# Performance work log

Measured on AMD Instinct MI355X. Metric: run time of the kernel, lower is better.

The kernel has to match this reference:

```python
import jax, jax.numpy as jnp
import numpy as np

PAD = 0
CONST_NO = 10000   # ids > CONST_NO are variables
N_PRED = 50
B, S, G = 8, 64, 8
F, R, BMAX = 200000, 200, 3
K_F, K_R = 64, 32  # max fact / rule children per state


def _is_var(x):
    return x > CONST_NO


def setup_inputs() -> dict:
    key = jax.random.key(0)
    ks = jax.random.split(key, 12)
    # facts: (pred, arg0, arg1), preds in [1, N_PRED], args are constants
    fp = jax.random.randint(ks[0], (F, 1), 1, N_PRED + 1, dtype=jnp.int32)
    fa = jax.random.randint(ks[1], (F, 2), 1, CONST_NO + 1, dtype=jnp.int32)
    facts = jnp.concatenate([fp, fa], axis=1)
    fact_scores = jax.random.uniform(ks[2], (F,), jnp.float32, 0.1, 1.0)
    # rule heads: p(V1, V2) with V1 = CONST_NO+1, V2 = CONST_NO+2
    hp = jax.random.randint(ks[3], (R, 1), 1, N_PRED + 1, dtype=jnp.int32)
    heads = jnp.concatenate([hp,
                             jnp.full((R, 1), CONST_NO + 1, jnp.int32),
                             jnp.full((R, 1), CONST_NO + 2, jnp.int32)], axis=1)
    # rule bodies: args are head vars or fresh constants
    bp = jax.random.randint(ks[4], (R, BMAX, 1), 1, N_PRED + 1, dtype=jnp.int32)
    choice = jax.random.randint(ks[5], (R, BMAX, 2), 0, 3, dtype=jnp.int32)
    consts = jax.random.randint(ks[6], (R, BMAX, 2), 1, CONST_NO + 1, dtype=jnp.int32)
    bargs = jnp.where(choice == 0, CONST_NO + 1,
                      jnp.where(choice == 1, CONST_NO + 2, consts)).astype(jnp.int32)
    bodies = jnp.concatenate([bp, bargs], axis=2)
    rule_lens = jax.random.randint(ks[7], (R,), 1, BMAX + 1, dtype=jnp.int32)
    rule_scores = jax.random.uniform(ks[8], (R,), jnp.float32, 0.1, 1.0)
    # proof goals [B,S,G,3]: args mix of constants and query vars CONST_NO+3/+4
    gp = jax.random.randint(ks[9], (B, S, G, 1), 1, N_PRED + 1, dtype=jnp.int32)
    vch = jax.random.randint(ks[10], (B, S, G, 2), 0, 4, dtype=jnp.int32)
    gc = jax.random.randint(ks[11], (B, S, G, 2), 1, CONST_NO + 1, dtype=jnp.int32)
    gargs = jnp.where(vch == 0, CONST_NO + 3,
                      jnp.where(vch == 1, CONST_NO + 4, gc)).astype(jnp.int32)
    goals = jnp.concatenate([gp, gargs], axis=3)
    # variable number of live goals per state (tail padded)
    pos = jnp.arange(G)
    keep = jax.random.randint(jax.random.fold_in(key, 99), (B, S, 1), 1, G + 1, dtype=jnp.int32)
    goals = jnp.where(pos[None, None, :, None] < keep[..., None], goals, PAD)
    state_scores = jax.random.uniform(jax.random.fold_in(key, 7), (B, S), jnp.float32, 0.1, 1.0)
    return dict(proof_goals=goals, state_scores=state_scores, facts=facts,
                fact_scores=fact_scores, heads=heads, bodies=bodies,
                rule_lens=rule_lens, rule_scores=rule_scores)


def reference(proof_goals, state_scores, facts, fact_scores, heads, bodies, rule_lens, rule_scores):
    # ---- 1. SELECT: query = goal slot 0, remaining goals mask slot 0 ----
    q = proof_goals[:, :, 0]                         # [B,S,3]
    active = q[..., 0] != PAD                        # [B,S]
    remaining = proof_goals.at[:, :, 0, :].set(PAD)  # [B,S,G,3]
    qp, qa0, qa1 = q[..., 0], q[..., 1], q[..., 2]

    # ---- 2. RESOLVE FACTS: unify query against fact table ----
    m = ((qp[..., None] == facts[:, 0])
         & (_is_var(qa0)[..., None] | (qa0[..., None] == facts[:, 1]))
         & (_is_var(qa1)[..., None] | (qa1[..., None] == facts[:, 2]))
         & active[..., None])                        # [B,S,F]
    fvals, fidx = jax.lax.top_k(m.astype(jnp.int32), K_F)
    fact_success = fvals > 0                         # [B,S,K_f]
    mf = facts[fidx]                                 # [B,S,K_f,3]
    # substitute query variables with matched fact constants in remaining goals
    v0 = qa0[:, :, None, None, None]
    v1 = qa1[:, :, None, None, None]
    b0 = mf[..., 1][..., None, None]
    b1 = mf[..., 2][..., None, None]
    rem = remaining[:, :, None]                      # [B,S,1,G,3]
    fg = jnp.where(_is_var(v0) & (rem == v0), b0, rem)
    fg = jnp.where(_is_var(v1) & (fg == v1), b1, fg)  # [B,S,K_f,G,3]
    fsc = jnp.where(fact_success, state_scores[:, :, None] * fact_scores[fidx], 0.0)

    # ---- 3. RESOLVE RULES: unify query against rule heads, append bodies ----
    mr = ((qp[..., None] == heads[:, 0])
          & (_is_var(heads[:, 1]) | _is_var(qa0)[..., None] | (qa0[..., None] == heads[:, 1]))
          & (_is_var(heads[:, 2]) | _is_var(qa1)[..., None] | (qa1[..., None] == heads[:, 2]))
          & active[..., None])                       # [B,S,R]
    rvals, ridx = jax.lax.top_k(mr.astype(jnp.int32), K_R)
    rule_success = rvals > 0                         # [B,S,K_r]
    mh = heads[ridx]                                 # [B,S,K_r,3]
    body = bodies[ridx]                              # [B,S,K_r,BMAX,3]
    h0 = mh[..., 1][..., None, None]
    h1 = mh[..., 2][..., None, None]
    qa0b = qa0[:, :, None, None, None]
    qa1b = qa1[:, :, None, None, None]
    body = jnp.where(_is_var(h0) & (body == h0), qa0b, body)
    body = jnp.where(_is_var(h1) & (body == h1), qa1b, body)
    bmask = jnp.arange(BMAX) < rule_lens[ridx][..., None]    # [B,S,K_r,BMAX]
    body = jnp.where(bmask[..., None], body, PAD)
    rem_rest = jnp.broadcast_to(remaining[:, :, None, 1:1 + (G - BMAX)], (B, S, K_R, G - BMAX, 3))
    rg = jnp.concatenate([body, rem_rest], axis=3)   # [B,S,K_r,G,3]
    rsc = jnp.where(rule_success, state_scores[:, :, None] * rule_scores[ridx], 0.0)

    # ---- 4. PACK: flatten SxK children, compact successful ones to S states ----
    K = K_F + K_R
    all_goals = jnp.concatenate([fg, rg], axis=2).reshape(B, S * K, G, 3)
    all_succ = jnp.concatenate([fact_success, rule_success], axis=2).reshape(B, S * K)
    all_sc = jnp.concatenate([fsc, rsc], axis=2).reshape(B, S * K)
    pvals, pidx = jax.lax.top_k(all_succ.astype(jnp.int32), S)
    new_succ = pvals > 0                             # [B,S]
    new_goals = jnp.take_along_axis(all_goals, pidx[..., None, None], axis=1)
    # ---- 5. POSTPROCESS: zero out failed / padded states ----
    new_goals = jnp.where(new_succ[..., None, None], new_goals, PAD)
    new_scores = jnp.where(new_succ, jnp.take_along_axis(all_sc, pidx, axis=1), 0.0)
    return new_goals, new_scores
```

## Files before the change

kernel.cpp:

```cpp
#include <hip/hip_runtime.h>

#define PAD 0
#define CONST_NO 10000
#define Bn 8
#define Sn 64
#define Gn 8
#define Fn 200000
#define Rn 200
#define BMAXn 3
#define KF 64
#define KR 32

#define NBLK 196
#define CHB  1024

#define OFF_CNTF   0
#define OFF_PN     512
#define OFF_PFIRST 1024
#define OFF_UF     5120

__device__ __forceinline__ bool isv(int x) { return x > CONST_NO; }

__global__ __launch_bounds__(256) void probe_kernel(
    const int* __restrict__ goals, const int* __restrict__ facts,
    int* __restrict__ ws)
{
    const int t = threadIdx.x;
    const int lane = t & 63, wv = t >> 6;

    if (blockIdx.x < NBLK) {
        __shared__ int4 qlist[512];
        __shared__ int qcnt[64], qstart[64];
        const int B = blockIdx.x;

        if (t < 64) qcnt[t] = 0;
        __syncthreads();

        int myPos[2], myQp[2], myQv[2], myQm[2], mySt[2];
        #pragma unroll
        for (int k = 0; k < 2; ++k) {
            const int s = t + k * 256;
            const int* q = goals + s * (Gn * 3);
            const int qp = q[0], qa0 = q[1], qa1 = q[2];
            const bool v0 = isv(qa0), v1 = isv(qa1);
            const bool use = (qp != PAD) && !(v0 && v1);
            myQp[k] = use ? qp : -1;
            myQv[k] = (v0 ? 0 : (qa0 << 14)) | (v1 ? 0 : qa1);
            myQm[k] = (v0 ? 0 : (0x3FFF << 14)) | (v1 ? 0 : 0x3FFF);
            mySt[k] = s;
            myPos[k] = use ? atomicAdd(&qcnt[qp], 1) : -1;
        }
        __syncthreads();
        if (t < 64) {
            const int v = qcnt[t];
            int incl = v;
            #pragma unroll
            for (int off = 1; off < 64; off <<= 1) {
                int n = __shfl_up(incl, off, 64);
                if (t >= off) incl += n;
            }
            qstart[t] = incl - v;
        }
        __syncthreads();
        #pragma unroll
        for (int k = 0; k < 2; ++k)
            if (myQp[k] >= 0)
                qlist[qstart[myQp[k]] + myPos[k]] =
                    make_int4(myQv[k], myQm[k], mySt[k], 0);
        __syncthreads();

        const int f0 = B * CHB + t * 4;
        int pv[4], pk[4];
        if (f0 + 3 < Fn) {
            const int4* p4 = (const int4*)(facts + 3 * f0);
            int4 a = p4[0], b4 = p4[1], c4 = p4[2];
            pv[0] = a.x;  pk[0] = (a.y  << 14) | a.z;
            pv[1] = a.w;  pk[1] = (b4.x << 14) | b4.y;
            pv[2] = b4.z; pk[2] = (b4.w << 14) | c4.x;
            pv[3] = c4.y; pk[3] = (c4.z << 14) | c4.w;
        } else {
            #pragma unroll
            for (int u = 0; u < 4; ++u) {
                pv[u] = -1; pk[u] = 0;
                if (f0 + u < Fn) {
                    pv[u] = facts[3 * (f0 + u)];
                    pk[u] = (facts[3 * (f0 + u) + 1] << 14) | facts[3 * (f0 + u) + 2];
                }
            }
        }
        #pragma unroll
        for (int u = 0; u < 4; ++u) {
            if (pv[u] >= 0) {
                const int j0 = qstart[pv[u]], j1 = j0 + qcnt[pv[u]];
                for (int j = j0; j < j1; ++j) {
                    const int4 qq = qlist[j];
                    if (((pk[u] ^ qq.x) & qq.y) == 0) {
                        const int pos = atomicAdd(ws + OFF_CNTF + qq.z, 1);
                        if (pos < KF) ws[OFF_UF + qq.z * KF + pos] = f0 + u;
                    }
                }
            }
        }
    } else {
        __shared__ int wave_tot[4];
        const int p = blockIdx.x - NBLK + 1;

        int total = 0;
        for (int base = 0; base < Fn && total < KF; base += 1024) {
            const int f0 = base + t * 4;
            unsigned mbits = 0;
            if (f0 + 3 < Fn) {
                const int4* p4 = (const int4*)(facts + 3 * f0);
                int4 a = p4[0], b4 = p4[1], c4 = p4[2];
                if (a.x  == p) mbits |= 1u;
                if (a.w  == p) mbits |= 2u;
                if (b4.z == p) mbits |= 4u;
                if (c4.y == p) mbits |= 8u;
            } else {
                #pragma unroll
                for (int u = 0; u < 4; ++u)
                    if (f0 + u < Fn && facts[3 * (f0 + u)] == p) mbits |= (1u << u);
            }
            const int c4n = __popc(mbits);

            int v = c4n;
            #pragma unroll
            for (int off = 1; off < 64; off <<= 1) {
                int n = __shfl_up(v, off, 64);
                if (lane >= off) v += n;
            }
            if (lane == 63) wave_tot[wv] = v;
            __syncthreads();
            int excl = v - c4n;
            #pragma unroll
            for (int w = 0; w < 4; ++w) if (w < wv) excl += wave_tot[w];
            const int ctot = wave_tot[0] + wave_tot[1] + wave_tot[2] + wave_tot[3];

            int pos = total + excl;
            #pragma unroll
            for (int u = 0; u < 4; ++u) {
                if (mbits & (1u << u)) {
                    if (pos < KF) ws[OFF_PFIRST + p * 64 + pos] = f0 + u;
                    pos++;
                }
            }
            total += ctot;
            __syncthreads();
        }
        if (t == 0) ws[OFF_PN + p] = (total < KF) ? total : KF;
    }
}

__global__ __launch_bounds__(256) void finalize_kernel(
    const int* __restrict__ goals, const float* __restrict__ ss,
    const int* __restrict__ facts, const float* __restrict__ fsc,
    const int* __restrict__ heads, const int* __restrict__ bodies,
    const int* __restrict__ rlens, const float* __restrict__ rsc,
    const int* __restrict__ ws, float* __restrict__ outp)
{
    __shared__ int sfx[Sn * 64];
    __shared__ int seg[4][Sn][16];
    __shared__ int segc[4][Sn];
    __shared__ int hds[Rn * 3];
    __shared__ int pref[Sn + 1];
    __shared__ int nfs[Sn], nrs[Sn], vvf[Sn], qps[Sn];

    const int b = blockIdx.x, t = threadIdx.x;
    const int lane = t & 63, wv = t >> 6;

    for (int k = t; k < Rn * 3; k += 256) hds[k] = heads[k];
    segc[wv][lane] = 0;
    __syncthreads();

    {
        const int s = lane;
        const int* q = goals + (b * Sn + s) * (Gn * 3);
        const int qp = q[0], qa0 = q[1], qa1 = q[2];
        const bool v0 = isv(qa0), v1 = isv(qa1);
        const bool active = (qp != PAD);
        int cnt = 0;
        const int r0 = wv * 50;
        for (int r = r0; r < r0 + 50; ++r) {
            const int h0 = hds[3 * r], h1 = hds[3 * r + 1], h2 = hds[3 * r + 2];
            if (active && h0 == qp && (isv(h1) || v0 || qa0 == h1)
                                   && (isv(h2) || v1 || qa1 == h2)) {
                if (cnt < 16) seg[wv][s][cnt] = r;
                cnt++;
            }
        }
        segc[wv][s] = (cnt < 16) ? cnt : 16;
    }
    __syncthreads();

    if (t < Sn) {
        const int s = t;
        const int* q = goals + (b * Sn + s) * (Gn * 3);
        const int qp = q[0], qa0 = q[1], qa1 = q[2];
        const bool v0 = isv(qa0), v1 = isv(qa1);
        const bool active = (qp != PAD);
        const bool vv = active && v0 && v1;
        int nf = 0;
        if (vv) {
            nf = ws[OFF_PN + qp];
        } else if (active) {
            int c = ws[OFF_CNTF + b * Sn + s];
            if (c > KF) c = KF;
            for (int j = 0; j < c; ++j)
                sfx[s * 64 + j] = ws[OFF_UF + (b * Sn + s) * KF + j];
            for (int a = 1; a < c; ++a) {
                const int key = sfx[s * 64 + a];
                int m = a - 1;
                while (m >= 0 && sfx[s * 64 + m] > key) {
                    sfx[s * 64 + m + 1] = sfx[s * 64 + m];
                    m--;
                }
                sfx[s * 64 + m + 1] = key;
            }
            nf = c;
        }
        nfs[s] = nf;
        vvf[s] = vv ? 1 : 0;
        qps[s] = qp;
        int nr = segc[0][s] + segc[1][s] + segc[2][s] + segc[3][s];
        if (nr > KR) nr = KR;
        nrs[s] = nr;

        int incl = nf + nr;
        #pragma unroll
        for (int off = 1; off < 64; off <<= 1) {
            int n = __shfl_up(incl, off, 64);
            if (t >= off) incl += n;
        }
        pref[s + 1] = incl;
        if (s == 0) pref[0] = 0;
    }
    __syncthreads();
    const int total = pref[Sn];

    for (int item = t; item < Sn * Gn; item += 256) {
        const int i = item >> 3, g = item & 7;
        int trip[3] = {PAD, PAD, PAD};
        if (i < total) {
            int lo = 0, hi = Sn - 1;
            while (lo < hi) {
                const int mid = (lo + hi) >> 1;
                if (pref[mid + 1] <= i) lo = mid + 1; else hi = mid;
            }
            const int s = lo, j = i - pref[s];
            const int* q = goals + (b * Sn + s) * (Gn * 3);
            const int qa0 = q[1], qa1 = q[2];
            if (j < nfs[s]) {
                const int fi = vvf[s] ? ws[OFF_PFIRST + qps[s] * 64 + j]
                                      : sfx[s * 64 + j];
                const int f1 = facts[3 * fi + 1], f2 = facts[3 * fi + 2];
                if (g >= 1) {
                    #pragma unroll
                    for (int c = 0; c < 3; ++c) {
                        int x = q[g * 3 + c];
                        if (isv(qa0) && x == qa0) x = f1;
                        else if (isv(qa1) && x == qa1) x = f2;
                        trip[c] = x;
                    }
                }
            } else {
                int jr = j - nfs[s];
                int wz = 0;
                while (jr >= segc[wz][s]) { jr -= segc[wz][s]; wz++; }
                const int ri = seg[wz][s][jr];
                const int h1 = hds[3 * ri + 1], h2 = hds[3 * ri + 2];
                const int len = rlens[ri];
                if (g < BMAXn) {
                    if (g < len) {
                        #pragma unroll
                        for (int c = 0; c < 3; ++c) {
                            int x = bodies[(ri * BMAXn + g) * 3 + c];
                            if (isv(h1) && x == h1) x = qa0;
                            if (isv(h2) && x == h2) x = qa1;
                            trip[c] = x;
                        }
                    }
                } else {
                    trip[0] = q[(g - 2) * 3 + 0];
                    trip[1] = q[(g - 2) * 3 + 1];
                    trip[2] = q[(g - 2) * 3 + 2];
                }
            }
        }
        float* o = outp + ((b * Sn + i) * Gn + g) * 3;
        o[0] = (float)trip[0];
        o[1] = (float)trip[1];
        o[2] = (float)trip[2];
    }

    if (t < Sn) {
        const int i = t;
        float sc = 0.f;
        if (i < total) {
            int lo = 0, hi = Sn - 1;
            while (lo < hi) {
                const int mid = (lo + hi) >> 1;
                if (pref[mid + 1] <= i) lo = mid + 1; else hi = mid;
            }
            const int s = lo, j = i - pref[s];
            const float stt = ss[b * Sn + s];
            if (j < nfs[s]) {
                const int fi = vvf[s] ? ws[OFF_PFIRST + qps[s] * 64 + j]
                                      : sfx[s * 64 + j];
                sc = stt * fsc[fi];
            } else {
                int jr = j - nfs[s];
                int wz = 0;
                while (jr >= segc[wz][s]) { jr -= segc[wz][s]; wz++; }
                sc = stt * rsc[seg[wz][s][jr]];
            }
        }
        outp[Bn * Sn * Gn * 3 + b * Sn + t] = sc;
    }
}

extern "C" void kernel_launch(void* const* d_in, const int* in_sizes, int n_in,
                              void* d_out, int out_size, void* d_ws, size_t ws_size,
                              hipStream_t stream) {
    const int*   goals  = (const int*)  d_in[0];
    const float* ss     = (const float*)d_in[1];
    const int*   facts  = (const int*)  d_in[2];
    const float* fsc    = (const float*)d_in[3];
    const int*   heads  = (const int*)  d_in[4];
    const int*   bodies = (const int*)  d_in[5];
    const int*   rlens  = (const int*)  d_in[6];
    const float* rsc    = (const float*)d_in[7];
    int*   ws   = (int*)d_ws;
    float* outp = (float*)d_out;

    hipMemsetAsync(ws, 0, 512 * sizeof(int), stream);
    probe_kernel   <<<NBLK + 50, 256, 0, stream>>>(goals, facts, ws);
    finalize_kernel<<<Bn,        256, 0, stream>>>(goals, ss, facts, fsc, heads,
                                                   bodies, rlens, rsc, ws, outp);
}
```

Before: 90.47 us.

## Fuse memset, probe and finalize into one cooperative kernel with grid syncs

Replaces the memset plus two kernel launches with a single cooperative kernel. The workspace counters are zeroed in-kernel and the probe and finalize phases are separated by grid.sync barriers. This is meant to remove launch overhead and the gaps between the three stream operations. In exchange it adds two grid-wide barriers and cooperative launch overhead, and it raises per-block shared memory because all phases' arrays now live in one kernel, which could limit occupancy.

```diff
diff --git a/kernel.cpp b/kernel.cpp
--- a/kernel.cpp
+++ b/kernel.cpp
@@ -1,4 +1,7 @@
 #include <hip/hip_runtime.h>
+#include <hip/hip_cooperative_groups.h>
+
+namespace cg = cooperative_groups;
 
 #define PAD 0
 #define CONST_NO 10000
@@ -21,16 +24,28 @@
 
 __device__ __forceinline__ bool isv(int x) { return x > CONST_NO; }
 
-__global__ __launch_bounds__(256) void probe_kernel(
-    const int* __restrict__ goals, const int* __restrict__ facts,
-    int* __restrict__ ws)
+__global__ __launch_bounds__(256) void fused_kernel(
+    const int* __restrict__ goals, const float* __restrict__ ss,
+    const int* __restrict__ facts, const float* __restrict__ fsc,
+    const int* __restrict__ heads, const int* __restrict__ bodies,
+    const int* __restrict__ rlens, const float* __restrict__ rsc,
+    int* __restrict__ ws, float* __restrict__ outp)
 {
+    cg::grid_group grid = cg::this_grid();
     const int t = threadIdx.x;
     const int lane = t & 63, wv = t >> 6;
 
+    {
+        const int gid = blockIdx.x * 256 + t;
+        if (gid < 512) ws[OFF_CNTF + gid] = 0;
+    }
+    grid.sync();
+
+    __shared__ int4 qlist[512];
+    __shared__ int qcnt[64], qstart[64];
+    __shared__ int wave_tot[4];
+
     if (blockIdx.x < NBLK) {
-        __shared__ int4 qlist[512];
-        __shared__ int qcnt[64], qstart[64];
         const int B = blockIdx.x;
 
         if (t < 64) qcnt[t] = 0;
@@ -102,7 +117,6 @@
             }
         }
     } else {
-        __shared__ int wave_tot[4];
         const int p = blockIdx.x - NBLK + 1;
 
         int total = 0;
@@ -149,172 +163,168 @@
         }
         if (t == 0) ws[OFF_PN + p] = (total < KF) ? total : KF;
     }
-}
-
-__global__ __launch_bounds__(256) void finalize_kernel(
-    const int* __restrict__ goals, const float* __restrict__ ss,
-    const int* __restrict__ facts, const float* __restrict__ fsc,
-    const int* __restrict__ heads, const int* __restrict__ bodies,
-    const int* __restrict__ rlens, const float* __restrict__ rsc,
-    const int* __restrict__ ws, float* __restrict__ outp)
-{
-    __shared__ int sfx[Sn * 64];
-    __shared__ int seg[4][Sn][16];
-    __shared__ int segc[4][Sn];
-    __shared__ int hds[Rn * 3];
-    __shared__ int pref[Sn + 1];
-    __shared__ int nfs[Sn], nrs[Sn], vvf[Sn], qps[Sn];
-
-    const int b = blockIdx.x, t = threadIdx.x;
-    const int lane = t & 63, wv = t >> 6;
-
-    for (int k = t; k < Rn * 3; k += 256) hds[k] = heads[k];
-    segc[wv][lane] = 0;
-    __syncthreads();
-
-    {
-        const int s = lane;
-        const int* q = goals + (b * Sn + s) * (Gn * 3);
-        const int qp = q[0], qa0 = q[1], qa1 = q[2];
-        const bool v0 = isv(qa0), v1 = isv(qa1);
-        const bool active = (qp != PAD);
-        int cnt = 0;
-        const int r0 = wv * 50;
-        for (int r = r0; r < r0 + 50; ++r) {
-            const int h0 = hds[3 * r], h1 = hds[3 * r + 1], h2 = hds[3 * r + 2];
-            if (active && h0 == qp && (isv(h1) || v0 || qa0 == h1)
-                                   && (isv(h2) || v1 || qa1 == h2)) {
-                if (cnt < 16) seg[wv][s][cnt] = r;
-                cnt++;
-            }
-        }
-        segc[wv][s] = (cnt < 16) ? cnt : 16;
-    }
-    __syncthreads();
-
-    if (t < Sn) {
-        const int s = t;
-        const int* q = goals + (b * Sn + s) * (Gn * 3);
-        const int qp = q[0], qa0 = q[1], qa1 = q[2];
-        const bool v0 = isv(qa0), v1 = isv(qa1);
-        const bool active = (qp != PAD);
-        const bool vv = active && v0 && v1;
-        int nf = 0;
-        if (vv) {
-            nf = ws[OFF_PN + qp];
-        } else if (active) {
-            int c = ws[OFF_CNTF + b * Sn + s];
-            if (c > KF) c = KF;
-            for (int j = 0; j < c; ++j)
-                sfx[s * 64 + j] = ws[OFF_UF + (b * Sn + s) * KF + j];
-            for (int a = 1; a < c; ++a) {
-                const int key = sfx[s * 64 + a];
-                int m = a - 1;
-                while (m >= 0 && sfx[s * 64 + m] > key) {
-                    sfx[s * 64 + m + 1] = sfx[s * 64 + m];
-                    m--;
-                }
-                sfx[s * 64 + m + 1] = key;
-            }
-            nf = c;
-        }
-        nfs[s] = nf;
-        vvf[s] = vv ? 1 : 0;
-        qps[s] = qp;
-        int nr = segc[0][s] + segc[1][s] + segc[2][s] + segc[3][s];
-        if (nr > KR) nr = KR;
-        nrs[s] = nr;
-
-        int incl = nf + nr;
-        #pragma unroll
-        for (int off = 1; off < 64; off <<= 1) {
-            int n = __shfl_up(incl, off, 64);
-            if (t >= off) incl += n;
-        }
-        pref[s + 1] = incl;
-        if (s == 0) pref[0] = 0;
-    }
-    __syncthreads();
-    const int total = pref[Sn];
-
-    for (int item = t; item < Sn * Gn; item += 256) {
-        const int i = item >> 3, g = item & 7;
-        int trip[3] = {PAD, PAD, PAD};
-        if (i < total) {
-            int lo = 0, hi = Sn - 1;
-            while (lo < hi) {
-                const int mid = (lo + hi) >> 1;
-                if (pref[mid + 1] <= i) lo = mid + 1; else hi = mid;
-            }
-            const int s = lo, j = i - pref[s];
+
+    __threadfence();
+    grid.sync();
+
+    if (blockIdx.x < Bn) {
+        __shared__ int sfx[Sn * 64];
+        __shared__ int seg[4][Sn][16];
+        __shared__ int segc[4][Sn];
+        __shared__ int hds[Rn * 3];
+        __shared__ int pref[Sn + 1];
+        __shared__ int nfs[Sn], nrs[Sn], vvf[Sn], qps[Sn];
+
+        const int b = blockIdx.x;
+
+        for (int k = t; k < Rn * 3; k += 256) hds[k] = heads[k];
+        segc[wv][lane] = 0;
+        __syncthreads();
+
+        {
+            const int s = lane;
             const int* q = goals + (b * Sn + s) * (Gn * 3);
-            const int qa0 = q[1], qa1 = q[2];
-            if (j < nfs[s]) {
-                const int fi = vvf[s] ? ws[OFF_PFIRST + qps[s] * 64 + j]
-                                      : sfx[s * 64 + j];
-                const int f1 = facts[3 * fi + 1], f2 = facts[3 * fi + 2];
-                if (g >= 1) {
-                    #pragma unroll
-                    for (int c = 0; c < 3; ++c) {
-                        int x = q[g * 3 + c];
-                        if (isv(qa0) && x == qa0) x = f1;
-                        else if (isv(qa1) && x == qa1) x = f2;
-                        trip[c] = x;
+            const int qp = q[0], qa0 = q[1], qa1 = q[2];
+            const bool v0 = isv(qa0), v1 = isv(qa1);
+            const bool active = (qp != PAD);
+            int cnt = 0;
+            const int r0 = wv * 50;
+            for (int r = r0; r < r0 + 50; ++r) {
+                const int h0 = hds[3 * r], h1 = hds[3 * r + 1], h2 = hds[3 * r + 2];
+                if (active && h0 == qp && (isv(h1) || v0 || qa0 == h1)
+                                       && (isv(h2) || v1 || qa1 == h2)) {
+                    if (cnt < 16) seg[wv][s][cnt] = r;
+                    cnt++;
+                }
+            }
+            segc[wv][s] = (cnt < 16) ? cnt : 16;
+        }
+        __syncthreads();
+
+        if (t < Sn) {
+            const int s = t;
+            const int* q = goals + (b * Sn + s) * (Gn * 3);
+            const int qp = q[0], qa0 = q[1], qa1 = q[2];
+            const bool v0 = isv(qa0), v1 = isv(qa1);
+            const bool active = (qp != PAD);
+            const bool vv = active && v0 && v1;
+            int nf = 0;
+            if (vv) {
+                nf = ws[OFF_PN + qp];
+            } else if (active) {
+                int c = ws[OFF_CNTF + b * Sn + s];
+                if (c > KF) c = KF;
+                for (int j = 0; j < c; ++j)
+                    sfx[s * 64 + j] = ws[OFF_UF + (b * Sn + s) * KF + j];
+                for (int a = 1; a < c; ++a) {
+                    const int key = sfx[s * 64 + a];
+                    int m = a - 1;
+                    while (m >= 0 && sfx[s * 64 + m] > key) {
+                        sfx[s * 64 + m + 1] = sfx[s * 64 + m];
+                        m--;
                     }
-                }
-            } else {
-                int jr = j - nfs[s];
-                int wz = 0;
-                while (jr >= segc[wz][s]) { jr -= segc[wz][s]; wz++; }
-                const int ri = seg[wz][s][jr];
-                const int h1 = hds[3 * ri + 1], h2 = hds[3 * ri + 2];
-                const int len = rlens[ri];
-                if (g < BMAXn) {
-                    if (g < len) {
+                    sfx[s * 64 + m + 1] = key;
+                }
+                nf = c;
+            }
+            nfs[s] = nf;
+            vvf[s] = vv ? 1 : 0;
+            qps[s] = qp;
+            int nr = segc[0][s] + segc[1][s] + segc[2][s] + segc[3][s];
+            if (nr > KR) nr = KR;
+            nrs[s] = nr;
+
+            int incl = nf + nr;
+            #pragma unroll
+            for (int off = 1; off < 64; off <<= 1) {
+                int n = __shfl_up(incl, off, 64);
+                if (t >= off) incl += n;
+            }
+            pref[s + 1] = incl;
+            if (s == 0) pref[0] = 0;
+        }
+        __syncthreads();
+        const int total = pref[Sn];
+
+        for (int item = t; item < Sn * Gn; item += 256) {
+            const int i = item >> 3, g = item & 7;
+            int trip[3] = {PAD, PAD, PAD};
+            if (i < total) {
+                int lo = 0, hi = Sn - 1;
+                while (lo < hi) {
+                    const int mid = (lo + hi) >> 1;
+                    if (pref[mid + 1] <= i) lo = mid + 1; else hi = mid;
+                }
+                const int s = lo, j = i - pref[s];
+                const int* q = goals + (b * Sn + s) * (Gn * 3);
+                const int qa0 = q[1], qa1 = q[2];
+                if (j < nfs[s]) {
+                    const int fi = vvf[s] ? ws[OFF_PFIRST + qps[s] * 64 + j]
+                                          : sfx[s * 64 + j];
+                    const int f1 = facts[3 * fi + 1], f2 = facts[3 * fi + 2];
+                    if (g >= 1) {
                         #pragma unroll
                         for (int c = 0; c < 3; ++c) {
-                            int x = bodies[(ri * BMAXn + g) * 3 + c];
-                            if (isv(h1) && x == h1) x = qa0;
-                            if (isv(h2) && x == h2) x = qa1;
+                            int x = q[g * 3 + c];
+                            if (isv(qa0) && x == qa0) x = f1;
+                            else if (isv(qa1) && x == qa1) x = f2;
                             trip[c] = x;
                         }
                     }
                 } else {
-                    trip[0] = q[(g - 2) * 3 + 0];
-                    trip[1] = q[(g - 2) * 3 + 1];
-                    trip[2] = q[(g - 2) * 3 + 2];
-                }
-            }
-        }
-        float* o = outp + ((b * Sn + i) * Gn + g) * 3;
-        o[0] = (float)trip[0];
-        o[1] = (float)trip[1];
-        o[2] = (float)trip[2];
-    }
-
-    if (t < Sn) {
-        const int i = t;
-        float sc = 0.f;
-        if (i < total) {
-            int lo = 0, hi = Sn - 1;
-            while (lo < hi) {
-                const int mid = (lo + hi) >> 1;
-                if (pref[mid + 1] <= i) lo = mid + 1; else hi = mid;
-            }
-            const int s = lo, j = i - pref[s];
-            const float stt = ss[b * Sn + s];
-            if (j < nfs[s]) {
-                const int fi = vvf[s] ? ws[OFF_PFIRST + qps[s] * 64 + j]
-                                      : sfx[s * 64 + j];
-                sc = stt * fsc[fi];
-            } else {
-                int jr = j - nfs[s];
-                int wz = 0;
-                while (jr >= segc[wz][s]) { jr -= segc[wz][s]; wz++; }
-                sc = stt * rsc[seg[wz][s][jr]];
-            }
-        }
-        outp[Bn * Sn * Gn * 3 + b * Sn + t] = sc;
+                    int jr = j - nfs[s];
+                    int wz = 0;
+                    while (jr >= segc[wz][s]) { jr -= segc[wz][s]; wz++; }
+                    const int ri = seg[wz][s][jr];
+                    const int h1 = hds[3 * ri + 1], h2 = hds[3 * ri + 2];
+                    const int len = rlens[ri];
+                    if (g < BMAXn) {
+                        if (g < len) {
+                            #pragma unroll
+                            for (int c = 0; c < 3; ++c) {
+                                int x = bodies[(ri * BMAXn + g) * 3 + c];
+                                if (isv(h1) && x == h1) x = qa0;
+                                if (isv(h2) && x == h2) x = qa1;
+                                trip[c] = x;
+                            }
+                        }
+                    } else {
+                        trip[0] = q[(g - 2) * 3 + 0];
+                        trip[1] = q[(g - 2) * 3 + 1];
+                        trip[2] = q[(g - 2) * 3 + 2];
+                    }
+                }
+            }
+            float* o = outp + ((b * Sn + i) * Gn + g) * 3;
+            o[0] = (float)trip[0];
+            o[1] = (float)trip[1];
+            o[2] = (float)trip[2];
+        }
+
+        if (t < Sn) {
+            const int i = t;
+            float sc = 0.f;
+            if (i < total) {
+                int lo = 0, hi = Sn - 1;
+                while (lo < hi) {
+                    const int mid = (lo + hi) >> 1;
+                    if (pref[mid + 1] <= i) lo = mid + 1; else hi = mid;
+                }
+                const int s = lo, j = i - pref[s];
+                const float stt = ss[b * Sn + s];
+                if (j < nfs[s]) {
+                    const int fi = vvf[s] ? ws[OFF_PFIRST + qps[s] * 64 + j]
+                                          : sfx[s * 64 + j];
+                    sc = stt * fsc[fi];
+                } else {
+                    int jr = j - nfs[s];
+                    int wz = 0;
+                    while (jr >= segc[wz][s]) { jr -= segc[wz][s]; wz++; }
+                    sc = stt * rsc[seg[wz][s][jr]];
+                }
+            }
+            outp[Bn * Sn * Gn * 3 + b * Sn + t] = sc;
+        }
     }
 }
 
@@ -332,8 +342,11 @@
     int*   ws   = (int*)d_ws;
     float* outp = (float*)d_out;
 
-    hipMemsetAsync(ws, 0, 512 * sizeof(int), stream);
-    probe_kernel   <<<NBLK + 50, 256, 0, stream>>>(goals, facts, ws);
-    finalize_kernel<<<Bn,        256, 0, stream>>>(goals, ss, facts, fsc, heads,
-                                                   bodies, rlens, rsc, ws, outp);
+    void* args[] = {
+        (void*)&goals, (void*)&ss, (void*)&facts, (void*)&fsc,
+        (void*)&heads, (void*)&bodies, (void*)&rlens, (void*)&rsc,
+        (void*)&ws, (void*)&outp
+    };
+    hipLaunchCooperativeKernel((void*)fused_kernel, dim3(NBLK + 50), dim3(256),
+                               args, 0, stream);
 }
```

Result: slower. 162.0 us (+79.0%).

## Build goal index once in setup kernel, replacing memset and per-block rebuild

Applied to the files above, without the earlier changes.

Goal bucketing (qlist/qstart/qcnt) used to be recomputed in every probe block; it is now built once by block 0 of a new setup kernel and stored in workspace. The same block zeroes the match counters, so the separate hipMemsetAsync is dropped. The per-predicate first-fact scan moves into the setup kernel. The probe kernel now just loads the prebuilt index. This removes redundant per-block shared-memory index building, but the probe must now wait for the setup kernel, so the first-fact scan no longer overlaps with probing.

```diff
diff --git a/kernel.cpp b/kernel.cpp
--- a/kernel.cpp
+++ b/kernel.cpp
@@ -18,21 +18,25 @@
 #define OFF_PN     512
 #define OFF_PFIRST 1024
 #define OFF_UF     5120
+#define OFF_QSTART 37888
+#define OFF_QCNT   37952
+#define OFF_QLIST  38016
 
 __device__ __forceinline__ bool isv(int x) { return x > CONST_NO; }
 
-__global__ __launch_bounds__(256) void probe_kernel(
+__global__ __launch_bounds__(256) void setup_kernel(
     const int* __restrict__ goals, const int* __restrict__ facts,
     int* __restrict__ ws)
 {
     const int t = threadIdx.x;
     const int lane = t & 63, wv = t >> 6;
 
-    if (blockIdx.x < NBLK) {
+    if (blockIdx.x == 0) {
+        ws[OFF_CNTF + t] = 0;
+        ws[OFF_CNTF + 256 + t] = 0;
+
         __shared__ int4 qlist[512];
         __shared__ int qcnt[64], qstart[64];
-        const int B = blockIdx.x;
-
         if (t < 64) qcnt[t] = 0;
         __syncthreads();
 
@@ -69,41 +73,16 @@
                     make_int4(myQv[k], myQm[k], mySt[k], 0);
         __syncthreads();
 
-        const int f0 = B * CHB + t * 4;
-        int pv[4], pk[4];
-        if (f0 + 3 < Fn) {
-            const int4* p4 = (const int4*)(facts + 3 * f0);
-            int4 a = p4[0], b4 = p4[1], c4 = p4[2];
-            pv[0] = a.x;  pk[0] = (a.y  << 14) | a.z;
-            pv[1] = a.w;  pk[1] = (b4.x << 14) | b4.y;
-            pv[2] = b4.z; pk[2] = (b4.w << 14) | c4.x;
-            pv[3] = c4.y; pk[3] = (c4.z << 14) | c4.w;
-        } else {
-            #pragma unroll
-            for (int u = 0; u < 4; ++u) {
-                pv[u] = -1; pk[u] = 0;
-                if (f0 + u < Fn) {
-                    pv[u] = facts[3 * (f0 + u)];
-                    pk[u] = (facts[3 * (f0 + u) + 1] << 14) | facts[3 * (f0 + u) + 2];
-                }
-            }
-        }
-        #pragma unroll
-        for (int u = 0; u < 4; ++u) {
-            if (pv[u] >= 0) {
-                const int j0 = qstart[pv[u]], j1 = j0 + qcnt[pv[u]];
-                for (int j = j0; j < j1; ++j) {
-                    const int4 qq = qlist[j];
-                    if (((pk[u] ^ qq.x) & qq.y) == 0) {
-                        const int pos = atomicAdd(ws + OFF_CNTF + qq.z, 1);
-                        if (pos < KF) ws[OFF_UF + qq.z * KF + pos] = f0 + u;
-                    }
-                }
-            }
-        }
+        if (t < 64) {
+            ws[OFF_QSTART + t] = qstart[t];
+            ws[OFF_QCNT + t]   = qcnt[t];
+        }
+        int4* dst = (int4*)(ws + OFF_QLIST);
+        dst[t]       = qlist[t];
+        dst[t + 256] = qlist[t + 256];
     } else {
         __shared__ int wave_tot[4];
-        const int p = blockIdx.x - NBLK + 1;
+        const int p = blockIdx.x;
 
         int total = 0;
         for (int base = 0; base < Fn && total < KF; base += 1024) {
@@ -151,6 +130,59 @@
     }
 }
 
+__global__ __launch_bounds__(256) void probe_kernel(
+    const int* __restrict__ facts, int* __restrict__ ws)
+{
+    __shared__ int4 qlist[512];
+    __shared__ int qstart[64], qcnt[64];
+    const int t = threadIdx.x;
+    const int B = blockIdx.x;
+
+    {
+        const int4* src = (const int4*)(ws + OFF_QLIST);
+        qlist[t]       = src[t];
+        qlist[t + 256] = src[t + 256];
+        if (t < 64) {
+            qstart[t] = ws[OFF_QSTART + t];
+            qcnt[t]   = ws[OFF_QCNT + t];
+        }
+    }
+    __syncthreads();
+
+    const int f0 = B * CHB + t * 4;
+    int pv[4], pk[4];
+    if (f0 + 3 < Fn) {
+        const int4* p4 = (const int4*)(facts + 3 * f0);
+        int4 a = p4[0], b4 = p4[1], c4 = p4[2];
+        pv[0] = a.x;  pk[0] = (a.y  << 14) | a.z;
+        pv[1] = a.w;  pk[1] = (b4.x << 14) | b4.y;
+        pv[2] = b4.z; pk[2] = (b4.w << 14) | c4.x;
+        pv[3] = c4.y; pk[3] = (c4.z << 14) | c4.w;
+    } else {
+        #pragma unroll
+        for (int u = 0; u < 4; ++u) {
+            pv[u] = -1; pk[u] = 0;
+            if (f0 + u < Fn) {
+                pv[u] = facts[3 * (f0 + u)];
+                pk[u] = (facts[3 * (f0 + u) + 1] << 14) | facts[3 * (f0 + u) + 2];
+            }
+        }
+    }
+    #pragma unroll
+    for (int u = 0; u < 4; ++u) {
+        if (pv[u] >= 0) {
+            const int j0 = qstart[pv[u]], j1 = j0 + qcnt[pv[u]];
+            for (int j = j0; j < j1; ++j) {
+                const int4 qq = qlist[j];
+                if (((pk[u] ^ qq.x) & qq.y) == 0) {
+                    const int pos = atomicAdd(ws + OFF_CNTF + qq.z, 1);
+                    if (pos < KF) ws[OFF_UF + qq.z * KF + pos] = f0 + u;
+                }
+            }
+        }
+    }
+}
+
 __global__ __launch_bounds__(256) void finalize_kernel(
     const int* __restrict__ goals, const float* __restrict__ ss,
     const int* __restrict__ facts, const float* __restrict__ fsc,
@@ -163,7 +195,7 @@
     __shared__ int segc[4][Sn];
     __shared__ int hds[Rn * 3];
     __shared__ int pref[Sn + 1];
-    __shared__ int nfs[Sn], nrs[Sn], vvf[Sn], qps[Sn];
+    __shared__ int nfs[Sn], vvf[Sn], qps[Sn];
 
     const int b = blockIdx.x, t = threadIdx.x;
     const int lane = t & 63, wv = t >> 6;
@@ -223,7 +255,6 @@
         qps[s] = qp;
         int nr = segc[0][s] + segc[1][s] + segc[2][s] + segc[3][s];
         if (nr > KR) nr = KR;
-        nrs[s] = nr;
 
         int incl = nf + nr;
         #pragma unroll
@@ -332,8 +363,8 @@
     int*   ws   = (int*)d_ws;
     float* outp = (float*)d_out;
 
-    hipMemsetAsync(ws, 0, 512 * sizeof(int), stream);
-    probe_kernel   <<<NBLK + 50, 256, 0, stream>>>(goals, facts, ws);
-    finalize_kernel<<<Bn,        256, 0, stream>>>(goals, ss, facts, fsc, heads,
-                                                   bodies, rlens, rsc, ws, outp);
+    setup_kernel   <<<51,   256, 0, stream>>>(goals, facts, ws);
+    probe_kernel   <<<NBLK, 256, 0, stream>>>(facts, ws);
+    finalize_kernel<<<Bn,   256, 0, stream>>>(goals, ss, facts, fsc, heads,
+                                              bodies, rlens, rsc, ws, outp);
 }
```

Result: slower. 96.31 us (+6.4%).

## Replace global atomic fact-match lists with per-block compacted buffers, drop memset

Applied to the files above, without the earlier changes.

The probe kernel no longer does a global atomicAdd per matching fact. Each block counts its matches, takes a block-wide prefix scan and writes packed (state, fact) entries into its own buffer region. The finalize kernel gathers all block buffers into shared memory, and each state scans the whole entry list to collect its facts in fact order. That ordering makes the insertion sort unnecessary. Removing the per-launch hipMemsetAsync drops one stream operation, but the match loop now runs twice and every state does a linear scan over up to 2048 entries.

```diff
diff --git a/kernel.cpp b/kernel.cpp
--- a/kernel.cpp
+++ b/kernel.cpp
@@ -13,11 +13,13 @@
 
 #define NBLK 196
 #define CHB  1024
-
-#define OFF_CNTF   0
-#define OFF_PN     512
-#define OFF_PFIRST 1024
-#define OFF_UF     5120
+#define CAP  1024
+#define ENTCAP 2048
+
+#define OFF_PN     0
+#define OFF_PFIRST 64
+#define OFF_BCNT   4160
+#define OFF_GBUF   4360
 
 __device__ __forceinline__ bool isv(int x) { return x > CONST_NO; }
 
@@ -31,12 +33,13 @@
     if (blockIdx.x < NBLK) {
         __shared__ int4 qlist[512];
         __shared__ int qcnt[64], qstart[64];
+        __shared__ int wtot[4];
         const int B = blockIdx.x;
 
         if (t < 64) qcnt[t] = 0;
         __syncthreads();
 
-        int myPos[2], myQp[2], myQv[2], myQm[2], mySt[2];
+        int myPos[2], myQp[2], myQv[2], myQm[2];
         #pragma unroll
         for (int k = 0; k < 2; ++k) {
             const int s = t + k * 256;
@@ -47,7 +50,6 @@
             myQp[k] = use ? qp : -1;
             myQv[k] = (v0 ? 0 : (qa0 << 14)) | (v1 ? 0 : qa1);
             myQm[k] = (v0 ? 0 : (0x3FFF << 14)) | (v1 ? 0 : 0x3FFF);
-            mySt[k] = s;
             myPos[k] = use ? atomicAdd(&qcnt[qp], 1) : -1;
         }
         __syncthreads();
@@ -66,7 +68,7 @@
         for (int k = 0; k < 2; ++k)
             if (myQp[k] >= 0)
                 qlist[qstart[myQp[k]] + myPos[k]] =
-                    make_int4(myQv[k], myQm[k], mySt[k], 0);
+                    make_int4(myQv[k], myQm[k], t + k * 256, 0);
         __syncthreads();
 
         const int f0 = B * CHB + t * 4;
@@ -88,15 +90,46 @@
                 }
             }
         }
+
+        int myCnt = 0;
         #pragma unroll
         for (int u = 0; u < 4; ++u) {
             if (pv[u] >= 0) {
                 const int j0 = qstart[pv[u]], j1 = j0 + qcnt[pv[u]];
                 for (int j = j0; j < j1; ++j) {
                     const int4 qq = qlist[j];
-                    if (((pk[u] ^ qq.x) & qq.y) == 0) {
-                        const int pos = atomicAdd(ws + OFF_CNTF + qq.z, 1);
-                        if (pos < KF) ws[OFF_UF + qq.z * KF + pos] = f0 + u;
+                    if (((pk[u] ^ qq.x) & qq.y) == 0) myCnt++;
+                }
+            }
+        }
+
+        int incl = myCnt;
+        #pragma unroll
+        for (int off = 1; off < 64; off <<= 1) {
+            int n = __shfl_up(incl, off, 64);
+            if (lane >= off) incl += n;
+        }
+        if (lane == 63) wtot[wv] = incl;
+        __syncthreads();
+        int excl = incl - myCnt;
+        #pragma unroll
+        for (int w = 0; w < 4; ++w) if (w < wv) excl += wtot[w];
+        const int btot = wtot[0] + wtot[1] + wtot[2] + wtot[3];
+        if (t == 0) ws[OFF_BCNT + B] = (btot < CAP) ? btot : CAP;
+
+        if (myCnt > 0) {
+            int* dst = ws + OFF_GBUF + B * CAP;
+            int k = excl;
+            #pragma unroll
+            for (int u = 0; u < 4; ++u) {
+                if (pv[u] >= 0) {
+                    const int j0 = qstart[pv[u]], j1 = j0 + qcnt[pv[u]];
+                    for (int j = j0; j < j1; ++j) {
+                        const int4 qq = qlist[j];
+                        if (((pk[u] ^ qq.x) & qq.y) == 0) {
+                            if (k < CAP) dst[k] = (qq.z << 18) | (f0 + u);
+                            k++;
+                        }
                     }
                 }
             }
@@ -163,14 +196,41 @@
     __shared__ int segc[4][Sn];
     __shared__ int hds[Rn * 3];
     __shared__ int pref[Sn + 1];
-    __shared__ int nfs[Sn], nrs[Sn], vvf[Sn], qps[Sn];
+    __shared__ int nfs[Sn], vvf[Sn], qps[Sn];
+    __shared__ int ent[ENTCAP];
+    __shared__ int bco[NBLK];
+    __shared__ int wsum[4];
 
     const int b = blockIdx.x, t = threadIdx.x;
     const int lane = t & 63, wv = t >> 6;
 
     for (int k = t; k < Rn * 3; k += 256) hds[k] = heads[k];
     segc[wv][lane] = 0;
+
+    const int bc = (t < NBLK) ? ws[OFF_BCNT + t] : 0;
+    int binc = bc;
+    #pragma unroll
+    for (int off = 1; off < 64; off <<= 1) {
+        int n = __shfl_up(binc, off, 64);
+        if (lane >= off) binc += n;
+    }
+    if (lane == 63) wsum[wv] = binc;
     __syncthreads();
+
+    int bexc = binc - bc;
+    #pragma unroll
+    for (int w = 0; w < 4; ++w) if (w < wv) bexc += wsum[w];
+    int TT = wsum[0] + wsum[1] + wsum[2] + wsum[3];
+    if (TT > ENTCAP) TT = ENTCAP;
+    if (t < NBLK) bco[t] = bexc;
+
+    if (t < NBLK) {
+        const int* src = ws + OFF_GBUF + t * CAP;
+        for (int k = 0; k < bc; ++k) {
+            const int o = bexc + k;
+            if (o < ENTCAP) ent[o] = src[k];
+        }
+    }
 
     {
         const int s = lane;
@@ -203,27 +263,21 @@
         if (vv) {
             nf = ws[OFF_PN + qp];
         } else if (active) {
-            int c = ws[OFF_CNTF + b * Sn + s];
-            if (c > KF) c = KF;
-            for (int j = 0; j < c; ++j)
-                sfx[s * 64 + j] = ws[OFF_UF + (b * Sn + s) * KF + j];
-            for (int a = 1; a < c; ++a) {
-                const int key = sfx[s * 64 + a];
-                int m = a - 1;
-                while (m >= 0 && sfx[s * 64 + m] > key) {
-                    sfx[s * 64 + m + 1] = sfx[s * 64 + m];
-                    m--;
-                }
-                sfx[s * 64 + m + 1] = key;
-            }
-            nf = c;
+            const int gs = b * Sn + s;
+            for (int j = 0; j < TT; ++j) {
+                const int e = ent[j];
+                if ((e >> 18) == gs) {
+                    if (nf < KF) sfx[s * 64 + nf] = e & 0x3FFFF;
+                    nf++;
+                }
+            }
+            if (nf > KF) nf = KF;
         }
         nfs[s] = nf;
         vvf[s] = vv ? 1 : 0;
         qps[s] = qp;
         int nr = segc[0][s] + segc[1][s] + segc[2][s] + segc[3][s];
         if (nr > KR) nr = KR;
-        nrs[s] = nr;
 
         int incl = nf + nr;
         #pragma unroll
@@ -332,7 +386,6 @@
     int*   ws   = (int*)d_ws;
     float* outp = (float*)d_out;
 
-    hipMemsetAsync(ws, 0, 512 * sizeof(int), stream);
     probe_kernel   <<<NBLK + 50, 256, 0, stream>>>(goals, facts, ws);
     finalize_kernel<<<Bn,        256, 0, stream>>>(goals, ss, facts, fsc, heads,
                                                    bodies, rlens, rsc, ws, outp);
```

Measured after the change: 95.81 us. +5.9%, slower.
